# Optimization experiments

Hardware: AMD Instinct MI355X
Metric: run time of the kernel (lower is better)

The kernel has to match this reference:

```python
import jax, jax.numpy as jnp
import numpy as np

N = 100000   # nodes per type
D = 128      # embedding_dim
H = 4        # attn_heads
C = D // H   # out_channels
E = 400000   # edges per relation
NEG_SLOPE = 0.01  # F.leaky_relu default


def setup_inputs() -> dict:
    key = jax.random.key(0)
    ks = jax.random.split(key, 24)
    inp = {
        "featA": jax.random.normal(ks[0], (N, D), jnp.float32),
        "featB": jax.random.normal(ks[1], (N, D), jnp.float32),
        "src_aa": jax.random.randint(ks[2], (E,), 0, N, jnp.int32),
        "dst_aa": jax.random.randint(ks[3], (E,), 0, N, jnp.int32),
        "src_ab": jax.random.randint(ks[4], (E,), 0, N, jnp.int32),
        "dst_ab": jax.random.randint(ks[5], (E,), 0, N, jnp.int32),
        "src_ba": jax.random.randint(ks[6], (E,), 0, N, jnp.int32),
        "dst_ba": jax.random.randint(ks[7], (E,), 0, N, jnp.int32),
    }
    # per-layer params: W stacked over node types [A=0, B=1]; attn over metapaths [aa=0, ab=1, ba=2]
    i = 8
    for t in range(2):
        inp[f"Wl{t}"] = jax.random.normal(ks[i + 0], (2, D, D), jnp.float32) * 0.05
        inp[f"bl{t}"] = jnp.zeros((2, D), jnp.float32)
        inp[f"Wr{t}"] = jax.random.normal(ks[i + 1], (2, D, D), jnp.float32) * 0.05
        inp[f"br{t}"] = jnp.zeros((2, D), jnp.float32)
        inp[f"al{t}"] = jax.random.normal(ks[i + 2], (3, H, C), jnp.float32) * 0.1
        inp[f"ar{t}"] = jax.random.normal(ks[i + 3], (3, H, C), jnp.float32) * 0.1
        i += 4
    return inp


def _segment_softmax(att, dst, n):
    # att: [E, H]; softmax over incoming edges per destination node, per head
    m = jax.ops.segment_max(att, dst, num_segments=n)
    e = jnp.exp(att - m[dst])
    s = jax.ops.segment_sum(e, dst, num_segments=n)
    return e / s[dst]


def _relation(k_src, v_dst, src, dst, a_l, a_r, n_dst):
    # per-edge attention: leaky_relu((k_src*attn_l).sum + (v_dst*attn_r).sum)
    att = jax.nn.leaky_relu((k_src[src] * a_l).sum(-1) + (v_dst[dst] * a_r).sum(-1), NEG_SLOPE)  # [E,H]
    alpha = _segment_softmax(att, dst, n_dst)                                                    # [E,H]
    # message h = v of the DESTINATION node (as in edge_attention), weighted-summed per dst
    h = jax.ops.segment_sum(alpha[..., None] * v_dst[dst], dst, num_segments=n_dst)              # [Nd,H,C]
    return h.reshape(n_dst, -1)


def _layer(hA, hB, Wl, bl, Wr, br, al, ar, edges):
    src_aa, dst_aa, src_ab, dst_ab, src_ba, dst_ba = edges
    kA = (hA @ Wl[0] + bl[0]).reshape(N, H, C)
    kB = (hB @ Wl[1] + bl[1]).reshape(N, H, C)
    vA = (hA @ Wr[0] + br[0]).reshape(N, H, C)
    vB = (hB @ Wr[1] + br[1]).reshape(N, H, C)
    h_aa = _relation(kA, vA, src_aa, dst_aa, al[0], ar[0], N)  # A -> A
    h_ab = _relation(kA, vB, src_ab, dst_ab, al[1], ar[1], N)  # A -> B
    h_ba = _relation(kB, vA, src_ba, dst_ba, al[2], ar[2], N)  # B -> A
    # mean over stacked relation outputs + the node's own v, then relu
    outA = jax.nn.relu((h_aa + h_ba + vA.reshape(N, D)) / 3.0)
    outB = jax.nn.relu((h_ab + vB.reshape(N, D)) / 2.0)
    return outA, outB


def reference(featA, featB, src_aa, dst_aa, src_ab, dst_ab, src_ba, dst_ba,
              Wl0, bl0, Wr0, br0, al0, ar0, Wl1, bl1, Wr1, br1, al1, ar1):
    edges = (src_aa, dst_aa, src_ab, dst_ab, src_ba, dst_ba)
    hA, hB = _layer(featA, featB, Wl0, bl0, Wr0, br0, al0, ar0, edges)
    hA, hB = _layer(hA, hB, Wl1, bl1, Wr1, br1, al1, ar1, edges)
    return jnp.stack([hA, hB])  # [2, N, D]
```

## Files before the change

### kernel.cpp

```cpp
#include <hip/hip_runtime.h>
#include <hip/hip_bf16.h>

#define NN 100000
#define EE 400000
#define NPAD 136

typedef unsigned short u16;
typedef __attribute__((ext_vector_type(4))) float floatx4;
typedef __attribute__((ext_vector_type(8))) short shortx8;

__device__ __forceinline__ u16 f2bf(float f) {
    unsigned u = __float_as_uint(f);
    u += 0x7FFFu + ((u >> 16) & 1u);
    return (u16)(u >> 16);
}

__global__ __launch_bounds__(256) void prep(
    const int* __restrict__ daa, const int* __restrict__ dab, const int* __restrict__ dba,
    unsigned char* __restrict__ masks,
    const float* __restrict__ Wr0, const float* __restrict__ Wr1,
    u16* __restrict__ Wt) {
    int b = blockIdx.x;
    int t = threadIdx.x;
    if (b < (EE + 255) / 256) {
        int e = b * 256 + t;
        if (e < EE) {
            masks[daa[e]] = 1;
            masks[NN + dab[e]] = 1;
            masks[2 * NN + dba[e]] = 1;
        }
    } else {
        int idx = (b - (EE + 255) / 256) * 256 + t;
        int mat = idx >> 14;
        int n = (idx >> 7) & 127;
        int k = idx & 127;
        const float* W = (mat < 2) ? (Wr0 + mat * 16384) : (Wr1 + (mat - 2) * 16384);
        Wt[idx] = f2bf(W[k * 128 + n]);
    }
}

__global__ __launch_bounds__(512, 4) void fused2(
    const float* __restrict__ featA, const float* __restrict__ featB,
    const u16* __restrict__ Wt,
    const float* __restrict__ br0, const float* __restrict__ br1,
    const unsigned char* __restrict__ masks,
    float* __restrict__ out) {
    __shared__ u16 ldsW0[128 * NPAD];
    __shared__ u16 ldsW1[128 * NPAD];

    const int blocksPerType = (NN + 127) / 128;
    const int type = (blockIdx.x >= blocksPerType) ? 1 : 0;
    const int blk = blockIdx.x - type * blocksPerType;
    const float* feat = type ? featB : featA;
    const u16* W0 = Wt + type * 16384;
    const u16* W1 = Wt + (2 + type) * 16384;
    const float* b0 = br0 + type * 128;
    const float* b1 = br1 + type * 128;
    float* outp = out + (size_t)type * NN * 128;

    const int t = threadIdx.x;
#pragma unroll
    for (int i = 0; i < 4; ++i) {
        int idx = i * 512 + t;
        int n = idx >> 4, c8 = idx & 15;
        *(shortx8*)&ldsW0[n * NPAD + c8 * 8] = ((const shortx8*)W0)[idx];
        *(shortx8*)&ldsW1[n * NPAD + c8 * 8] = ((const shortx8*)W1)[idx];
    }

    const int wave = t >> 6;
    const int lane = t & 63;
    const int quad = lane >> 4;
    const int mrow = lane & 15;
    const int m0 = blk * 128 + wave * 16;
    const int m = m0 + mrow;
    const int msafe = (m < NN) ? m : (NN - 1);

    shortx8 afrag[4];
    {
        const float* arow = feat + (size_t)msafe * 128;
#pragma unroll
        for (int ks = 0; ks < 4; ++ks) {
            floatx4 f0 = *(const floatx4*)(arow + ks * 32 + quad * 8);
            floatx4 f1 = *(const floatx4*)(arow + ks * 32 + quad * 8 + 4);
            union { shortx8 v; u16 u[8]; } uu;
            uu.u[0] = f2bf(f0[0]); uu.u[1] = f2bf(f0[1]);
            uu.u[2] = f2bf(f0[2]); uu.u[3] = f2bf(f0[3]);
            uu.u[4] = f2bf(f1[0]); uu.u[5] = f2bf(f1[1]);
            uu.u[6] = f2bf(f1[2]); uu.u[7] = f2bf(f1[3]);
            afrag[ks] = uu.v;
        }
    }

    float scl[4];
#pragma unroll
    for (int r = 0; r < 4; ++r) {
        int rr = m0 + quad * 4 + r;
        rr = (rr < NN) ? rr : (NN - 1);
        scl[r] = type ? (1.0f + (float)masks[NN + rr]) * 0.5f
                      : (1.0f + (float)masks[rr] + (float)masks[2 * NN + rr]) * (1.0f / 3.0f);
    }

    __syncthreads();

    floatx4 acc[8];
#pragma unroll
    for (int nt = 0; nt < 8; ++nt) acc[nt] = (floatx4){0.f, 0.f, 0.f, 0.f};
#pragma unroll
    for (int ks = 0; ks < 4; ++ks)
#pragma unroll
        for (int nt = 0; nt < 8; ++nt) {
            shortx8 bfr = *(const shortx8*)&ldsW0[(nt * 16 + mrow) * NPAD + ks * 32 + quad * 8];
            acc[nt] = __builtin_amdgcn_mfma_f32_16x16x32_bf16(afrag[ks], bfr, acc[nt], 0, 0, 0);
        }

    __syncthreads();

#pragma unroll
    for (int nt = 0; nt < 8; ++nt) {
        int col = nt * 16 + mrow;
        float bv = b0[col];
#pragma unroll
        for (int r = 0; r < 4; ++r) {
            float v = fmaxf((acc[nt][r] + bv) * scl[r], 0.0f);
            ldsW0[(wave * 16 + quad * 4 + r) * NPAD + col] = f2bf(v);
        }
    }
    __syncthreads();

    shortx8 a2[4];
#pragma unroll
    for (int ks = 0; ks < 4; ++ks)
        a2[ks] = *(const shortx8*)&ldsW0[(wave * 16 + mrow) * NPAD + ks * 32 + quad * 8];

    floatx4 acc2[8];
#pragma unroll
    for (int nt = 0; nt < 8; ++nt) acc2[nt] = (floatx4){0.f, 0.f, 0.f, 0.f};
#pragma unroll
    for (int ks = 0; ks < 4; ++ks)
#pragma unroll
        for (int nt = 0; nt < 8; ++nt) {
            shortx8 bfr = *(const shortx8*)&ldsW1[(nt * 16 + mrow) * NPAD + ks * 32 + quad * 8];
            acc2[nt] = __builtin_amdgcn_mfma_f32_16x16x32_bf16(a2[ks], bfr, acc2[nt], 0, 0, 0);
        }

#pragma unroll
    for (int nt = 0; nt < 8; ++nt) {
        int col = nt * 16 + mrow;
        float bv = b1[col];
#pragma unroll
        for (int r = 0; r < 4; ++r) {
            int row = m0 + quad * 4 + r;
            if (row < NN)
                outp[(size_t)row * 128 + col] = fmaxf((acc2[nt][r] + bv) * scl[r], 0.0f);
        }
    }
}

extern "C" void kernel_launch(void* const* d_in, const int* in_sizes, int n_in,
                              void* d_out, int out_size, void* d_ws, size_t ws_size,
                              hipStream_t stream) {
    (void)in_sizes; (void)n_in; (void)out_size; (void)ws_size;
    const float* featA = (const float*)d_in[0];
    const float* featB = (const float*)d_in[1];
    const int* dst_aa = (const int*)d_in[3];
    const int* dst_ab = (const int*)d_in[5];
    const int* dst_ba = (const int*)d_in[7];
    const float* Wr0 = (const float*)d_in[10];
    const float* br0 = (const float*)d_in[11];
    const float* Wr1 = (const float*)d_in[16];
    const float* br1 = (const float*)d_in[17];

    char* ws = (char*)d_ws;
    u16* Wt = (u16*)ws;
    unsigned char* masks = (unsigned char*)(ws + 4 * 16384 * 2);

    hipMemsetAsync(masks, 0, (size_t)3 * NN, stream);
    const int markBlocks = (EE + 255) / 256;
    prep<<<markBlocks + 256, 256, 0, stream>>>(dst_aa, dst_ab, dst_ba, masks, Wr0, Wr1, Wt);

    const int blocksPerType = (NN + 127) / 128;
    fused2<<<2 * blocksPerType, 512, 0, stream>>>(featA, featB, Wt, br0, br1, masks,
                                                  (float*)d_out);
}
```

Baseline: 253.9 us.

## Pre-swizzle weights into MFMA fragment order, transpose tiles for vector stores, bitmask masks

The prep kernel now writes the bf16 weights already in MFMA fragment order, so the fused kernel copies them into LDS linearly and reads contiguous per-lane fragments with no padding. The MFMA operands are swapped so each lane owns one output row. That gives one scale per lane, float4 bias loads, per-wave LDS staging of the intermediate without a block barrier, and row-contiguous float4 output stores in place of scattered scalar writes. The per-node destination masks become atomicOr bitmasks, which shrinks the memset and the mask reads but adds atomic contention during marking.

```diff
diff --git a/kernel.cpp b/kernel.cpp
--- a/kernel.cpp
+++ b/kernel.cpp
@@ -3,11 +3,13 @@
 
 #define NN 100000
 #define EE 400000
-#define NPAD 136
+#define EBLK ((EE + 255) / 256)
 
 typedef unsigned short u16;
+typedef unsigned int u32;
 typedef __attribute__((ext_vector_type(4))) float floatx4;
 typedef __attribute__((ext_vector_type(8))) short shortx8;
+typedef __attribute__((ext_vector_type(4))) unsigned short ushortx4;
 
 __device__ __forceinline__ u16 f2bf(float f) {
     unsigned u = __float_as_uint(f);
@@ -17,67 +19,64 @@
 
 __global__ __launch_bounds__(256) void prep(
     const int* __restrict__ daa, const int* __restrict__ dab, const int* __restrict__ dba,
-    unsigned char* __restrict__ masks,
+    u32* __restrict__ bm,
     const float* __restrict__ Wr0, const float* __restrict__ Wr1,
-    u16* __restrict__ Wt) {
-    int b = blockIdx.x;
-    int t = threadIdx.x;
-    if (b < (EE + 255) / 256) {
+    u16* __restrict__ Wtf) {
+    int b = blockIdx.x, t = threadIdx.x;
+    if (b < EBLK) {
         int e = b * 256 + t;
         if (e < EE) {
-            masks[daa[e]] = 1;
-            masks[NN + dab[e]] = 1;
-            masks[2 * NN + dba[e]] = 1;
+            int d0 = daa[e], d1 = dab[e], d2 = dba[e];
+            atomicOr(&bm[d0 >> 5], 1u << (d0 & 31));
+            atomicOr(&bm[3200 + (d1 >> 5)], 1u << (d1 & 31));
+            atomicOr(&bm[6400 + (d2 >> 5)], 1u << (d2 & 31));
         }
     } else {
-        int idx = (b - (EE + 255) / 256) * 256 + t;
+        int idx = (b - EBLK) * 256 + t;
         int mat = idx >> 14;
-        int n = (idx >> 7) & 127;
-        int k = idx & 127;
+        int fidx = idx & 16383;
+        int chunk = fidx >> 9;
+        int lane = (fidx >> 3) & 63;
+        int j = fidx & 7;
+        int k = (chunk >> 3) * 32 + ((lane >> 4) & 3) * 8 + j;
+        int n = (chunk & 7) * 16 + (lane & 15);
         const float* W = (mat < 2) ? (Wr0 + mat * 16384) : (Wr1 + (mat - 2) * 16384);
-        Wt[idx] = f2bf(W[k * 128 + n]);
+        Wtf[idx] = f2bf(W[k * 128 + n]);
     }
 }
 
 __global__ __launch_bounds__(512, 4) void fused2(
     const float* __restrict__ featA, const float* __restrict__ featB,
-    const u16* __restrict__ Wt,
+    const u16* __restrict__ Wtf, const u32* __restrict__ bm,
     const float* __restrict__ br0, const float* __restrict__ br1,
-    const unsigned char* __restrict__ masks,
     float* __restrict__ out) {
-    __shared__ u16 ldsW0[128 * NPAD];
-    __shared__ u16 ldsW1[128 * NPAD];
+    __shared__ u16 lds[32768];
 
-    const int blocksPerType = (NN + 127) / 128;
-    const int type = (blockIdx.x >= blocksPerType) ? 1 : 0;
-    const int blk = blockIdx.x - type * blocksPerType;
+    const int type = (blockIdx.x >= 782) ? 1 : 0;
+    const int blk = blockIdx.x - type * 782;
     const float* feat = type ? featB : featA;
-    const u16* W0 = Wt + type * 16384;
-    const u16* W1 = Wt + (2 + type) * 16384;
+    const u16* W0g = Wtf + type * 16384;
+    const u16* W1g = Wtf + (2 + type) * 16384;
     const float* b0 = br0 + type * 128;
     const float* b1 = br1 + type * 128;
     float* outp = out + (size_t)type * NN * 128;
 
     const int t = threadIdx.x;
+    const int wave = t >> 6, lane = t & 63;
+    const int quad = lane >> 4, mrow = lane & 15;
+    const int row = blk * 128 + wave * 16 + mrow;
+    const int rc = (row < NN) ? row : (NN - 1);
+
 #pragma unroll
     for (int i = 0; i < 4; ++i) {
-        int idx = i * 512 + t;
-        int n = idx >> 4, c8 = idx & 15;
-        *(shortx8*)&ldsW0[n * NPAD + c8 * 8] = ((const shortx8*)W0)[idx];
-        *(shortx8*)&ldsW1[n * NPAD + c8 * 8] = ((const shortx8*)W1)[idx];
+        int off = (i * 512 + t) * 8;
+        *(shortx8*)&lds[off] = *(const shortx8*)&W0g[off];
+        *(shortx8*)&lds[16384 + off] = *(const shortx8*)&W1g[off];
     }
 
-    const int wave = t >> 6;
-    const int lane = t & 63;
-    const int quad = lane >> 4;
-    const int mrow = lane & 15;
-    const int m0 = blk * 128 + wave * 16;
-    const int m = m0 + mrow;
-    const int msafe = (m < NN) ? m : (NN - 1);
-
-    shortx8 afrag[4];
+    shortx8 bfrag[4];
     {
-        const float* arow = feat + (size_t)msafe * 128;
+        const float* arow = feat + (size_t)rc * 128;
 #pragma unroll
         for (int ks = 0; ks < 4; ++ks) {
             floatx4 f0 = *(const floatx4*)(arow + ks * 32 + quad * 8);
@@ -87,17 +86,21 @@
             uu.u[2] = f2bf(f0[2]); uu.u[3] = f2bf(f0[3]);
             uu.u[4] = f2bf(f1[0]); uu.u[5] = f2bf(f1[1]);
             uu.u[6] = f2bf(f1[2]); uu.u[7] = f2bf(f1[3]);
-            afrag[ks] = uu.v;
+            bfrag[ks] = uu.v;
         }
     }
 
-    float scl[4];
-#pragma unroll
-    for (int r = 0; r < 4; ++r) {
-        int rr = m0 + quad * 4 + r;
-        rr = (rr < NN) ? rr : (NN - 1);
-        scl[r] = type ? (1.0f + (float)masks[NN + rr]) * 0.5f
-                      : (1.0f + (float)masks[rr] + (float)masks[2 * NN + rr]) * (1.0f / 3.0f);
+    float scl;
+    {
+        int w = rc >> 5, s = rc & 31;
+        if (type) {
+            float ab = (float)((bm[3200 + w] >> s) & 1u);
+            scl = (1.0f + ab) * 0.5f;
+        } else {
+            float aa = (float)((bm[w] >> s) & 1u);
+            float ba = (float)((bm[6400 + w] >> s) & 1u);
+            scl = (1.0f + aa + ba) * (1.0f / 3.0f);
+        }
     }
 
     __syncthreads();
@@ -109,28 +112,29 @@
     for (int ks = 0; ks < 4; ++ks)
 #pragma unroll
         for (int nt = 0; nt < 8; ++nt) {
-            shortx8 bfr = *(const shortx8*)&ldsW0[(nt * 16 + mrow) * NPAD + ks * 32 + quad * 8];
-            acc[nt] = __builtin_amdgcn_mfma_f32_16x16x32_bf16(afrag[ks], bfr, acc[nt], 0, 0, 0);
+            shortx8 af = *(const shortx8*)&lds[((ks * 8 + nt) << 9) + lane * 8];
+            acc[nt] = __builtin_amdgcn_mfma_f32_16x16x32_bf16(af, bfrag[ks], acc[nt], 0, 0, 0);
         }
 
     __syncthreads();
 
+    const int h1base = wave * 2048;
 #pragma unroll
     for (int nt = 0; nt < 8; ++nt) {
-        int col = nt * 16 + mrow;
-        float bv = b0[col];
+        floatx4 bv = *(const floatx4*)(b0 + nt * 16 + quad * 4);
+        ushortx4 p;
 #pragma unroll
-        for (int r = 0; r < 4; ++r) {
-            float v = fmaxf((acc[nt][r] + bv) * scl[r], 0.0f);
-            ldsW0[(wave * 16 + quad * 4 + r) * NPAD + col] = f2bf(v);
-        }
+        for (int r = 0; r < 4; ++r)
+            p[r] = f2bf(fmaxf((acc[nt][r] + bv[r]) * scl, 0.0f));
+        int q2 = (2 * nt + (quad >> 1)) & 3;
+        int addr = h1base + (nt >> 1) * 512 + q2 * 128 + mrow * 8 + (quad & 1) * 4;
+        *(ushortx4*)&lds[addr] = p;
     }
-    __syncthreads();
 
-    shortx8 a2[4];
+    shortx8 h1b[4];
 #pragma unroll
     for (int ks = 0; ks < 4; ++ks)
-        a2[ks] = *(const shortx8*)&ldsW0[(wave * 16 + mrow) * NPAD + ks * 32 + quad * 8];
+        h1b[ks] = *(const shortx8*)&lds[h1base + ks * 512 + lane * 8];
 
     floatx4 acc2[8];
 #pragma unroll
@@ -139,19 +143,20 @@
     for (int ks = 0; ks < 4; ++ks)
 #pragma unroll
         for (int nt = 0; nt < 8; ++nt) {
-            shortx8 bfr = *(const shortx8*)&ldsW1[(nt * 16 + mrow) * NPAD + ks * 32 + quad * 8];
-            acc2[nt] = __builtin_amdgcn_mfma_f32_16x16x32_bf16(a2[ks], bfr, acc2[nt], 0, 0, 0);
+            shortx8 af = *(const shortx8*)&lds[16384 + ((ks * 8 + nt) << 9) + lane * 8];
+            acc2[nt] = __builtin_amdgcn_mfma_f32_16x16x32_bf16(af, h1b[ks], acc2[nt], 0, 0, 0);
         }
 
+    if (row < NN) {
+        float* orow = outp + (size_t)row * 128;
 #pragma unroll
-    for (int nt = 0; nt < 8; ++nt) {
-        int col = nt * 16 + mrow;
-        float bv = b1[col];
+        for (int nt = 0; nt < 8; ++nt) {
+            floatx4 bv = *(const floatx4*)(b1 + nt * 16 + quad * 4);
+            floatx4 o;
 #pragma unroll
-        for (int r = 0; r < 4; ++r) {
-            int row = m0 + quad * 4 + r;
-            if (row < NN)
-                outp[(size_t)row * 128 + col] = fmaxf((acc2[nt][r] + bv) * scl[r], 0.0f);
+            for (int r = 0; r < 4; ++r)
+                o[r] = fmaxf((acc2[nt][r] + bv[r]) * scl, 0.0f);
+            *(floatx4*)(orow + nt * 16 + quad * 4) = o;
         }
     }
 }
@@ -171,14 +176,10 @@
     const float* br1 = (const float*)d_in[17];
 
     char* ws = (char*)d_ws;
-    u16* Wt = (u16*)ws;
-    unsigned char* masks = (unsigned char*)(ws + 4 * 16384 * 2);
+    u16* Wtf = (u16*)ws;
+    u32* bm = (u32*)(ws + 131072);
 
-    hipMemsetAsync(masks, 0, (size_t)3 * NN, stream);
-    const int markBlocks = (EE + 255) / 256;
-    prep<<<markBlocks + 256, 256, 0, stream>>>(dst_aa, dst_ab, dst_ba, masks, Wr0, Wr1, Wt);
-
-    const int blocksPerType = (NN + 127) / 128;
-    fused2<<<2 * blocksPerType, 512, 0, stream>>>(featA, featB, Wt, br0, br1, masks,
-                                                  (float*)d_out);
+    hipMemsetAsync(bm, 0, 3 * 3200 * sizeof(u32), stream);
+    prep<<<EBLK + 256, 256, 0, stream>>>(dst_aa, dst_ab, dst_ba, bm, Wr0, Wr1, Wtf);
+    fused2<<<2 * 782, 512, 0, stream>>>(featA, featB, Wtf, bm, br0, br1, (float*)d_out);
 }
```

After: 302.8 us. +19.3%, slower.
